# Kernel optimization log

Measured on AMD Instinct MI355X. Metric: run time of the kernel, lower is better.

## Reference

```python
import jax, jax.numpy as jnp
import numpy as np

N_NODES = 50000
N_EDGES = 800000
D = 128


def setup_inputs() -> dict:
    key = jax.random.key(0)
    ks = jax.random.split(key, 7)
    return {
        "shape_features": jax.random.normal(ks[0], (N_NODES, D), dtype=jnp.float32),
        "W1": jax.random.normal(ks[1], (D, D), dtype=jnp.float32) * 0.05,
        "b1": jax.random.normal(ks[2], (D,), dtype=jnp.float32) * 0.05,
        "W2": jax.random.normal(ks[3], (D, D), dtype=jnp.float32) * 0.05,
        "b2": jax.random.normal(ks[4], (D,), dtype=jnp.float32) * 0.05,
        "edge_src": jax.random.randint(ks[5], (N_EDGES,), 0, N_NODES, dtype=jnp.int32),
        "edge_dst": jax.random.randint(ks[6], (N_EDGES,), 0, N_NODES, dtype=jnp.int32),
    }


def reference(shape_features, W1, b1, W2, b2, edge_src, edge_dst):
    # out1 = linear1(x)  (torch Linear: x @ W.T + b)
    out1 = jnp.einsum("nd,od->no", shape_features, W1) + b1
    # ragged neighbour gather + sum per destination node (segment reduce)
    aggr = jax.ops.segment_sum(shape_features[edge_src], edge_dst,
                               num_segments=shape_features.shape[0])
    # out = linear1(x) + linear2(aggr)
    return out1 + jnp.einsum("nd,od->no", aggr, W2) + b2
```

## Files before the change

kernel.cpp:

```cpp
#include <hip/hip_runtime.h>
#include <hip/hip_bf16.h>

#define DF 128
#define BSH 5
#define BNODES 32
#define NBMAX 2048
#define PCHUNK 8192
#define BCHUNK 4096
#define TILE 2048
#define ASTRIDE 68
#define SRCMASK 0x07ffffffu

typedef __attribute__((ext_vector_type(8))) short short8;
typedef __attribute__((ext_vector_type(4))) float floatx4;

__device__ __forceinline__ ushort f2bf(float f) {
    __hip_bfloat16 h = __float2bfloat16(f);
    return *reinterpret_cast<ushort*>(&h);
}

__global__ __launch_bounds__(256) void prep_kernel(
    const float* __restrict__ x, ushort* __restrict__ xbf, int n4,
    const float* __restrict__ W1, const float* __restrict__ W2,
    const float* __restrict__ b1, const float* __restrict__ b2,
    ushort* __restrict__ w1bf, ushort* __restrict__ w2bf, float* __restrict__ bias,
    const int* __restrict__ dst, int* __restrict__ ghist, int* __restrict__ done,
    int* __restrict__ gbase, int* __restrict__ gcur,
    int n_edges, int PH, int nb)
{
    __shared__ int h[NBMAX];
    __shared__ int isLast;
    int bid = blockIdx.x;
    if (bid < PH) {
        for (int j = threadIdx.x; j < nb; j += 256) h[j] = 0;
        __syncthreads();
        int base = bid * PCHUNK;
#pragma unroll 4
        for (int i = 0; i < PCHUNK / 256; ++i) {
            int e = base + i * 256 + threadIdx.x;
            if (e < n_edges) atomicAdd(&h[dst[e] >> BSH], 1);
        }
        __syncthreads();
        for (int j = threadIdx.x; j < nb; j += 256) {
            int c = h[j];
            if (c) atomicAdd(&ghist[j], c);
        }
        __threadfence();
        __syncthreads();
        if (threadIdx.x == 0) isLast = (atomicAdd(done, 1) == PH - 1);
        __syncthreads();
        if (isLast) {
            int b0 = threadIdx.x * 8;
            int vals[8];
            int s = 0;
#pragma unroll
            for (int k = 0; k < 8; ++k) {
                int idx = b0 + k;
                int v = (idx < nb)
                    ? __hip_atomic_load(&ghist[idx], __ATOMIC_RELAXED,
                                        __HIP_MEMORY_SCOPE_AGENT)
                    : 0;
                vals[k] = v; s += v;
            }
            h[threadIdx.x] = s;
            __syncthreads();
            for (int off = 1; off < 256; off <<= 1) {
                int u = (threadIdx.x >= off) ? h[threadIdx.x - off] : 0;
                __syncthreads();
                h[threadIdx.x] += u;
                __syncthreads();
            }
            int run = h[threadIdx.x] - s;
#pragma unroll
            for (int k = 0; k < 8; ++k) {
                int idx = b0 + k;
                if (idx < nb) { gbase[idx] = run; gcur[idx] = run; run += vals[k]; }
            }
            if (threadIdx.x == 0) gbase[nb] = n_edges;
        }
    } else if (bid < PH + 64) {
        int i = (bid - PH) * 256 + threadIdx.x;
        if (i < DF * DF) {
            w1bf[i] = f2bf(W1[i]);
            w2bf[i] = f2bf(W2[i]);
        }
        if (i < DF) bias[i] = b1[i] + b2[i];
    } else {
        int i = (bid - PH - 64) * 256 + threadIdx.x;
        if (i < n4) {
            float4 v = reinterpret_cast<const float4*>(x)[i];
            ushort4 o;
            o.x = f2bf(v.x); o.y = f2bf(v.y); o.z = f2bf(v.z); o.w = f2bf(v.w);
            reinterpret_cast<ushort4*>(xbf)[i] = o;
        }
    }
}

__global__ __launch_bounds__(512) void bin_kernel(
    const int* __restrict__ src, const int* __restrict__ dst,
    int* __restrict__ gcur, uint* __restrict__ pairs, int n_edges, int nb)
{
    __shared__ int h[NBMAX];
    int tid = threadIdx.x;
    for (int j = tid; j < nb; j += 512) h[j] = 0;
    __syncthreads();
    int base = blockIdx.x * BCHUNK;
    int d[8], sv[8];
#pragma unroll
    for (int k = 0; k < 8; ++k) {
        int i = base + k * 512 + tid;
        bool ok = i < n_edges;
        d[k]  = ok ? dst[i] : -1;
        sv[k] = ok ? src[i] : 0;
        if (ok) atomicAdd(&h[d[k] >> BSH], 1);
    }
    __syncthreads();
    for (int j = tid; j < nb; j += 512) {
        int c = h[j];
        if (c) h[j] = atomicAdd(&gcur[j], c);
    }
    __syncthreads();
#pragma unroll
    for (int k = 0; k < 8; ++k) {
        if (d[k] >= 0) {
            int p = atomicAdd(&h[d[k] >> BSH], 1);
            pairs[p] = (uint)sv[k] | ((uint)(d[k] & (BNODES - 1)) << 27);
        }
    }
}

__global__ __launch_bounds__(256, 6) void agg_gemm_kernel(
    const ushort* __restrict__ xbf, const uint* __restrict__ pairs,
    const int* __restrict__ gbase,
    const ushort* __restrict__ w1, const ushort* __restrict__ w2,
    const float* __restrict__ bias, float* __restrict__ out, int n_nodes)
{
    __shared__ uint sorted[TILE];
    __shared__ uint abuf[BNODES * ASTRIDE];
    __shared__ int hcnt[BNODES];
    __shared__ int hoff[BNODES + 1];
    __shared__ int hcur[BNODES];

    int blk   = blockIdx.x;
    int node0 = blk * BNODES;
    int wave  = threadIdx.x >> 6;
    int lane  = threadIdx.x & 63;

    int start = gbase[blk];
    int end   = gbase[blk + 1];

    const char* xu = (const char*)xbf;
    uint lane4 = (uint)lane << 2;

    float2 acc[8];
#pragma unroll
    for (int i = 0; i < 8; ++i) acc[i] = make_float2(0.f, 0.f);

    for (int t0 = start; t0 < end; t0 += TILE) {
        int cnt = end - t0; if (cnt > TILE) cnt = TILE;

        if (threadIdx.x < BNODES) hcnt[threadIdx.x] = 0;
        __syncthreads();

        uint pk_[8];
#pragma unroll
        for (int k = 0; k < 8; ++k) {
            int i = threadIdx.x + k * 256;
            if (i < cnt) {
                uint pk = pairs[t0 + i];
                pk_[k] = pk;
                atomicAdd(&hcnt[pk >> 27], 1);
            }
        }
        __syncthreads();

        if (threadIdx.x < 64) {
            int v = (lane < BNODES) ? hcnt[lane] : 0;
#pragma unroll
            for (int off = 1; off < BNODES; off <<= 1) {
                int u = __shfl_up(v, off);
                if (lane >= off) v += u;
            }
            if (lane < BNODES) {
                hoff[lane + 1] = v;
                hcur[lane] = v - hcnt[lane];
            }
            if (lane == 0) hoff[0] = 0;
        }
        __syncthreads();

#pragma unroll
        for (int k = 0; k < 8; ++k) {
            int i = threadIdx.x + k * 256;
            if (i < cnt) {
                uint pk = pk_[k];
                int p = atomicAdd(&hcur[pk >> 27], 1);
                sorted[p] = (pk & SRCMASK) << 8;
            }
        }
        __syncthreads();

#pragma unroll
        for (int i = 0; i < 8; ++i) {
            int nl = wave * 8 + i;
            int j0 = hoff[nl], j1 = hoff[nl + 1];
            float2 a = acc[i];
            int j = j0;
            for (; j + 15 < j1; j += 16) {
                uint u[16];
#pragma unroll
                for (int k = 0; k < 16; ++k)
                    u[k] = *(const uint*)(xu + (size_t)(sorted[j + k] + lane4));
#pragma unroll
                for (int k = 0; k < 16; ++k) {
                    a.x += __uint_as_float(u[k] << 16);
                    a.y += __uint_as_float(u[k] & 0xffff0000u);
                }
            }
            for (; j + 3 < j1; j += 4) {
                uint u0 = *(const uint*)(xu + (size_t)(sorted[j + 0] + lane4));
                uint u1 = *(const uint*)(xu + (size_t)(sorted[j + 1] + lane4));
                uint u2 = *(const uint*)(xu + (size_t)(sorted[j + 2] + lane4));
                uint u3 = *(const uint*)(xu + (size_t)(sorted[j + 3] + lane4));
                a.x += __uint_as_float(u0 << 16) + __uint_as_float(u1 << 16)
                     + __uint_as_float(u2 << 16) + __uint_as_float(u3 << 16);
                a.y += __uint_as_float(u0 & 0xffff0000u) + __uint_as_float(u1 & 0xffff0000u)
                     + __uint_as_float(u2 & 0xffff0000u) + __uint_as_float(u3 & 0xffff0000u);
            }
            for (; j < j1; ++j) {
                uint u = *(const uint*)(xu + (size_t)(sorted[j] + lane4));
                a.x += __uint_as_float(u << 16);
                a.y += __uint_as_float(u & 0xffff0000u);
            }
            acc[i] = a;
        }
        __syncthreads();
    }

#pragma unroll
    for (int i = 0; i < 8; ++i) {
        int nl = wave * 8 + i;
        abuf[nl * ASTRIDE + lane] =
            (uint)f2bf(acc[i].x) | ((uint)f2bf(acc[i].y) << 16);
    }
    __syncthreads();

    int quad = lane >> 4;
    int m    = lane & 15;
    int rg   = wave >> 1;
    int half = wave & 1;
    int rowL = rg * 16 + m;
    int rowG = node0 + rowL;
    int rowC = (rowG < n_nodes) ? rowG : (n_nodes - 1);

    short8 xa[4], aa[4];
#pragma unroll
    for (int ks = 0; ks < 4; ++ks) {
        xa[ks] = *reinterpret_cast<const short8*>(xbf + (size_t)rowC * DF + ks * 32 + quad * 8);
        aa[ks] = *reinterpret_cast<const short8*>(&abuf[rowL * ASTRIDE + ks * 16 + quad * 4]);
    }

    int nbase = node0 + rg * 16;
#pragma unroll
    for (int oi = 0; oi < 4; ++oi) {
        int ot = half * 4 + oi;
        int o = ot * 16 + m;
        floatx4 c = {0.f, 0.f, 0.f, 0.f};
#pragma unroll
        for (int ks = 0; ks < 4; ++ks) {
            short8 bf1 = *reinterpret_cast<const short8*>(w1 + (size_t)o * DF + ks * 32 + quad * 8);
            short8 bf2 = *reinterpret_cast<const short8*>(w2 + (size_t)o * DF + ks * 32 + quad * 8);
            c = __builtin_amdgcn_mfma_f32_16x16x32_bf16(xa[ks], bf1, c, 0, 0, 0);
            c = __builtin_amdgcn_mfma_f32_16x16x32_bf16(aa[ks], bf2, c, 0, 0, 0);
        }
        float bv = bias[o];
#pragma unroll
        for (int r = 0; r < 4; ++r) {
            int row = nbase + quad * 4 + r;
            if (row < n_nodes) out[(size_t)row * DF + o] = c[r] + bv;
        }
    }
}

extern "C" void kernel_launch(void* const* d_in, const int* in_sizes, int n_in,
                              void* d_out, int out_size, void* d_ws, size_t ws_size,
                              hipStream_t stream) {
    const float* x  = (const float*)d_in[0];
    const float* W1 = (const float*)d_in[1];
    const float* b1 = (const float*)d_in[2];
    const float* W2 = (const float*)d_in[3];
    const float* b2 = (const float*)d_in[4];
    const int* esrc = (const int*)d_in[5];
    const int* edst = (const int*)d_in[6];
    float* out = (float*)d_out;

    int n_nodes = in_sizes[0] / DF;
    int n_edges = in_sizes[5];

    int nb = (n_nodes + BNODES - 1) >> BSH;
    int PH = (n_edges + PCHUNK - 1) / PCHUNK;
    int BB = (n_edges + BCHUNK - 1) / BCHUNK;

    char* ws = (char*)d_ws;
    ushort* xbf   = (ushort*)ws;                 ws += (size_t)n_nodes * DF * 2;
    ushort* w1bf  = (ushort*)ws;                 ws += (size_t)DF * DF * 2;
    ushort* w2bf  = (ushort*)ws;                 ws += (size_t)DF * DF * 2;
    float*  bias  = (float*)ws;                  ws += (size_t)DF * 4;
    int*    ghist = (int*)ws;                    ws += (size_t)(nb + 1) * 4;
    int*    done  = ghist + nb;
    int*    gbase = (int*)ws;                    ws += (size_t)(nb + 1) * 4;
    int*    gcur  = (int*)ws;                    ws += (size_t)nb * 4;
    uint*   pairs = (uint*)ws;

    hipMemsetAsync(ghist, 0, (size_t)(nb + 1) * sizeof(int), stream);

    int n4 = n_nodes * DF / 4;
    int prep_blocks = PH + 64 + (n4 + 255) / 256;
    prep_kernel<<<prep_blocks, 256, 0, stream>>>(
        x, xbf, n4, W1, W2, b1, b2, w1bf, w2bf, bias,
        edst, ghist, done, gbase, gcur, n_edges, PH, nb);

    bin_kernel<<<BB, 512, 0, stream>>>(esrc, edst, gcur, pairs, n_edges, nb);

    agg_gemm_kernel<<<nb, 256, 0, stream>>>(
        xbf, pairs, gbase, w1bf, w2bf, bias, out, n_nodes);
}
```

Baseline: 188.1 us.

## Two-level radix binning of edges and interleaved 4-node gather loop

Replaces the single scatter pass over 1563 fine bins with a two-level sort. The prep kernel first buckets edges into 49 coarse 1024-node chunks through a shared-memory staging buffer. A second kernel then sorts each chunk into 32 fine bins, so the scattered global writes become more coalesced. The aggregation loop now processes four nodes at once in batches of 8 with predicated loads, which raises memory-level parallelism at the cost of some wasted loads. Risks: src is packed into 16 bits (needs n_nodes < 65536), CAPC caps the per-chunk capacity, and NC_ is hardcoded to the node count.

```diff
diff --git a/kernel.cpp b/kernel.cpp
--- a/kernel.cpp
+++ b/kernel.cpp
@@ -5,8 +5,12 @@
 #define BSH 5
 #define BNODES 32
 #define NBMAX 2048
-#define PCHUNK 8192
-#define BCHUNK 4096
+#define CSH 10
+#define NC_ 49
+#define CAPC 24576
+#define PCHUNK 4096
+#define CHUNKB 4096
+#define KMAX 6
 #define TILE 2048
 #define ASTRIDE 68
 #define SRCMASK 0x07ffffffu
@@ -19,42 +23,96 @@
     return *reinterpret_cast<ushort*>(&h);
 }
 
-__global__ __launch_bounds__(256) void prep_kernel(
+__global__ __launch_bounds__(512) void prep_kernel(
     const float* __restrict__ x, ushort* __restrict__ xbf, int n4,
     const float* __restrict__ W1, const float* __restrict__ W2,
     const float* __restrict__ b1, const float* __restrict__ b2,
     ushort* __restrict__ w1bf, ushort* __restrict__ w2bf, float* __restrict__ bias,
-    const int* __restrict__ dst, int* __restrict__ ghist, int* __restrict__ done,
-    int* __restrict__ gbase, int* __restrict__ gcur,
-    int n_edges, int PH, int nb)
+    const int* __restrict__ src, const int* __restrict__ dst,
+    int* __restrict__ ghist, int* __restrict__ done, int* __restrict__ gcurC,
+    uint* __restrict__ stagingC, int* __restrict__ gbase, int* __restrict__ gcurF,
+    int n_edges, int EB, int WB, int nb)
 {
-    __shared__ int h[NBMAX];
-    __shared__ int isLast;
+    __shared__ int  hf[NBMAX];
+    __shared__ int  hc[NC_];
+    __shared__ int  lcur[NC_];
+    __shared__ int  wb[NC_];
+    __shared__ uint stg[PCHUNK];
+    __shared__ int  isLast;
+
     int bid = blockIdx.x;
-    if (bid < PH) {
-        for (int j = threadIdx.x; j < nb; j += 256) h[j] = 0;
-        __syncthreads();
+    int tid = threadIdx.x;
+
+    if (bid < EB) {
         int base = bid * PCHUNK;
-#pragma unroll 4
-        for (int i = 0; i < PCHUNK / 256; ++i) {
-            int e = base + i * 256 + threadIdx.x;
-            if (e < n_edges) atomicAdd(&h[dst[e] >> BSH], 1);
-        }
-        __syncthreads();
-        for (int j = threadIdx.x; j < nb; j += 256) {
-            int c = h[j];
+        int cnt = n_edges - base; if (cnt > PCHUNK) cnt = PCHUNK;
+
+        for (int j = tid; j < nb; j += 512) hf[j] = 0;
+        if (tid < NC_) hc[tid] = 0;
+        __syncthreads();
+#pragma unroll
+        for (int k = 0; k < PCHUNK / 512; ++k) {
+            int i = k * 512 + tid;
+            if (i < cnt) {
+                int d = dst[base + i];
+                atomicAdd(&hf[d >> BSH], 1);
+                atomicAdd(&hc[d >> CSH], 1);
+            }
+        }
+        __syncthreads();
+        for (int j = tid; j < nb; j += 512) {
+            int c = hf[j];
             if (c) atomicAdd(&ghist[j], c);
         }
+        if (tid < 64) {
+            int c = (tid < NC_) ? hc[tid] : 0;
+            int s = c;
+#pragma unroll
+            for (int off = 1; off < 64; off <<= 1) {
+                int u = __shfl_up(s, off);
+                if (tid >= off) s += u;
+            }
+            if (tid < NC_) {
+                int excl = s - c;
+                lcur[tid] = excl;
+                int gp = 0;
+                if (c > 0) gp = atomicAdd(&gcurC[tid], c);
+                wb[tid] = tid * CAPC + gp - excl;
+            }
+        }
+        __syncthreads();
+#pragma unroll
+        for (int k = 0; k < PCHUNK / 512; ++k) {
+            int i = k * 512 + tid;
+            if (i < cnt) {
+                int e = base + i;
+                int d = dst[e];
+                int c = d >> CSH;
+                uint pk = (uint)src[e] | ((uint)(d & 1023) << 16) | ((uint)c << 26);
+                int p = atomicAdd(&lcur[c], 1);
+                stg[p] = pk;
+            }
+        }
+        __syncthreads();
+#pragma unroll
+        for (int k = 0; k < PCHUNK / 512; ++k) {
+            int i = k * 512 + tid;
+            if (i < cnt) {
+                uint pk = stg[i];
+                int c = (int)(pk >> 26);
+                stagingC[wb[c] + i] = pk;
+            }
+        }
         __threadfence();
         __syncthreads();
-        if (threadIdx.x == 0) isLast = (atomicAdd(done, 1) == PH - 1);
+        if (tid == 0) isLast = (atomicAdd(done, 1) == EB - 1);
         __syncthreads();
         if (isLast) {
-            int b0 = threadIdx.x * 8;
-            int vals[8];
+            int b0 = tid * 4;
+            int vals[4];
             int s = 0;
 #pragma unroll
-            for (int k = 0; k < 8; ++k) {
+            for (int k = 0; k < 4; ++k) {
                 int idx = b0 + k;
                 int v = (idx < nb)
                     ? __hip_atomic_load(&ghist[idx], __ATOMIC_RELAXED,
@@ -62,31 +120,31 @@
                     : 0;
                 vals[k] = v; s += v;
             }
-            h[threadIdx.x] = s;
+            hf[tid] = s;
             __syncthreads();
-            for (int off = 1; off < 256; off <<= 1) {
-                int u = (threadIdx.x >= off) ? h[threadIdx.x - off] : 0;
+            for (int off = 1; off < 512; off <<= 1) {
+                int u = (tid >= off) ? hf[tid - off] : 0;
                 __syncthreads();
-                h[threadIdx.x] += u;
+                hf[tid] += u;
                 __syncthreads();
             }
-            int run = h[threadIdx.x] - s;
-#pragma unroll
-            for (int k = 0; k < 8; ++k) {
+            int run = hf[tid] - s;
+#pragma unroll
+            for (int k = 0; k < 4; ++k) {
                 int idx = b0 + k;
-                if (idx < nb) { gbase[idx] = run; gcur[idx] = run; run += vals[k]; }
-            }
-            if (threadIdx.x == 0) gbase[nb] = n_edges;
-        }
-    } else if (bid < PH + 64) {
-        int i = (bid - PH) * 256 + threadIdx.x;
+                if (idx < nb) { gbase[idx] = run; gcurF[idx] = run; run += vals[k]; }
+            }
+            if (tid == 0) gbase[nb] = n_edges;
+        }
+    } else if (bid < EB + WB) {
+        int i = (bid - EB) * 512 + tid;
         if (i < DF * DF) {
             w1bf[i] = f2bf(W1[i]);
             w2bf[i] = f2bf(W2[i]);
         }
         if (i < DF) bias[i] = b1[i] + b2[i];
     } else {
-        int i = (bid - PH - 64) * 256 + threadIdx.x;
+        int i = (bid - EB - WB) * 512 + tid;
         if (i < n4) {
             float4 v = reinterpret_cast<const float4*>(x)[i];
             ushort4 o;
@@ -96,35 +154,75 @@
     }
 }
 
-__global__ __launch_bounds__(512) void bin_kernel(
-    const int* __restrict__ src, const int* __restrict__ dst,
-    int* __restrict__ gcur, uint* __restrict__ pairs, int n_edges, int nb)
+__global__ __launch_bounds__(512) void binB_kernel(
+    const uint* __restrict__ stagingC, const int* __restrict__ gcurC,
+    int* __restrict__ gcurF, uint* __restrict__ pairs)
 {
-    __shared__ int h[NBMAX];
+    __shared__ uint stg[CHUNKB];
+    __shared__ int h32[BNODES];
+    __shared__ int lcur[BNODES];
+    __shared__ int wb[BNODES];
+
+    int c = blockIdx.x / KMAX;
+    int k = blockIdx.x % KMAX;
     int tid = threadIdx.x;
-    for (int j = tid; j < nb; j += 512) h[j] = 0;
+
+    int size = gcurC[c];
+    if (size > CAPC) size = CAPC;
+    int s0 = k * CHUNKB;
+    if (s0 >= size) return;
+    int cnt = size - s0; if (cnt > CHUNKB) cnt = CHUNKB;
+    const uint* sp = stagingC + (size_t)c * CAPC + s0;
+
+    if (tid < BNODES) h32[tid] = 0;
     __syncthreads();
-    int base = blockIdx.x * BCHUNK;
-    int d[8], sv[8];
-#pragma unroll
-    for (int k = 0; k < 8; ++k) {
-        int i = base + k * 512 + tid;
-        bool ok = i < n_edges;
-        d[k]  = ok ? dst[i] : -1;
-        sv[k] = ok ? src[i] : 0;
-        if (ok) atomicAdd(&h[d[k] >> BSH], 1);
+
+    uint mypk[CHUNKB / 512];
+#pragma unroll
+    for (int q = 0; q < CHUNKB / 512; ++q) {
+        int i = q * 512 + tid;
+        if (i < cnt) {
+            uint pk = sp[i];
+            mypk[q] = pk;
+            atomicAdd(&h32[(pk >> 21) & 31], 1);
+        }
     }
     __syncthreads();
-    for (int j = tid; j < nb; j += 512) {
-        int c = h[j];
-        if (c) h[j] = atomicAdd(&gcur[j], c);
+    if (tid < 64) {
+        int v = (tid < BNODES) ? h32[tid] : 0;
+        int s = v;
+#pragma unroll
+        for (int off = 1; off < BNODES; off <<= 1) {
+            int u = __shfl_up(s, off);
+            if (tid >= off) s += u;
+        }
+        if (tid < BNODES) {
+            int excl = s - v;
+            lcur[tid] = excl;
+            int gp = 0;
+            if (v > 0) gp = atomicAdd(&gcurF[c * BNODES + tid], v);
+            wb[tid] = gp - excl;
+        }
     }
     __syncthreads();
 #pragma unroll
-    for (int k = 0; k < 8; ++k) {
-        if (d[k] >= 0) {
-            int p = atomicAdd(&h[d[k] >> BSH], 1);
-            pairs[p] = (uint)sv[k] | ((uint)(d[k] & (BNODES - 1)) << 27);
+    for (int q = 0; q < CHUNKB / 512; ++q) {
+        int i = q * 512 + tid;
+        if (i < cnt) {
+            uint pk = mypk[q];
+            int p = atomicAdd(&lcur[(pk >> 21) & 31], 1);
+            stg[p] = pk;
+        }
+    }
+    __syncthreads();
+#pragma unroll
+    for (int q = 0; q < CHUNKB / 512; ++q) {
+        int i = q * 512 + tid;
+        if (i < cnt) {
+            uint pk = stg[i];
+            int f = (int)((pk >> 21) & 31);
+            uint out = (pk & 0xFFFFu) | (((pk >> 16) & 31u) << 27);
+            pairs[wb[f] + i] = out;
         }
     }
 }
@@ -200,39 +298,55 @@
         }
         __syncthreads();
 
-#pragma unroll
-        for (int i = 0; i < 8; ++i) {
-            int nl = wave * 8 + i;
-            int j0 = hoff[nl], j1 = hoff[nl + 1];
-            float2 a = acc[i];
-            int j = j0;
-            for (; j + 15 < j1; j += 16) {
-                uint u[16];
-#pragma unroll
-                for (int k = 0; k < 16; ++k)
-                    u[k] = *(const uint*)(xu + (size_t)(sorted[j + k] + lane4));
-#pragma unroll
-                for (int k = 0; k < 16; ++k) {
-                    a.x += __uint_as_float(u[k] << 16);
-                    a.y += __uint_as_float(u[k] & 0xffff0000u);
+        int hv[9];
+#pragma unroll
+        for (int q = 0; q <= 8; ++q) hv[q] = hoff[wave * 8 + q];
+        int safe = hv[0];
+#pragma unroll
+        for (int g = 0; g < 2; ++g) {
+            int j0 = hv[g * 4 + 0], e0 = hv[g * 4 + 1];
+            int j1 = e0,            e1 = hv[g * 4 + 2];
+            int j2 = e1,            e2 = hv[g * 4 + 3];
+            int j3 = e2,            e3 = hv[g * 4 + 4];
+            int rem = e0 - j0;
+            rem = max(rem, e1 - j1);
+            rem = max(rem, e2 - j2);
+            rem = max(rem, e3 - j3);
+            float2 a0 = acc[g * 4 + 0], a1 = acc[g * 4 + 1];
+            float2 a2 = acc[g * 4 + 2], a3 = acc[g * 4 + 3];
+            while (rem > 0) {
+                uint u0[8], u1[8], u2[8], u3[8];
+#pragma unroll
+                for (int k = 0; k < 8; ++k) {
+                    int i0 = (j0 + k < e0) ? j0 + k : safe;
+                    int i1 = (j1 + k < e1) ? j1 + k : safe;
+                    int i2 = (j2 + k < e2) ? j2 + k : safe;
+                    int i3 = (j3 + k < e3) ? j3 + k : safe;
+                    u0[k] = *(const uint*)(xu + (size_t)(sorted[i0] + lane4));
+                    u1[k] = *(const uint*)(xu + (size_t)(sorted[i1] + lane4));
+                    u2[k] = *(const uint*)(xu + (size_t)(sorted[i2] + lane4));
+                    u3[k] = *(const uint*)(xu + (size_t)(sorted[i3] + lane4));
                 }
-            }
-            for (; j + 3 < j1; j += 4) {
-                uint u0 = *(const uint*)(xu + (size_t)(sorted[j + 0] + lane4));
-                uint u1 = *(const uint*)(xu + (size_t)(sorted[j + 1] + lane4));
-                uint u2 = *(const uint*)(xu + (size_t)(sorted[j + 2] + lane4));
-                uint u3 = *(const uint*)(xu + (size_t)(sorted[j + 3] + lane4));
-                a.x += __uint_as_float(u0 << 16) + __uint_as_float(u1 << 16)
-                     + __uint_as_float(u2 << 16) + __uint_as_float(u3 << 16);
-                a.y += __uint_as_float(u0 & 0xffff0000u) + __uint_as_float(u1 & 0xffff0000u)
-                     + __uint_as_float(u2 & 0xffff0000u) + __uint_as_float(u3 & 0xffff0000u);
-            }
-            for (; j < j1; ++j) {
-                uint u = *(const uint*)(xu + (size_t)(sorted[j] + lane4));
-                a.x += __uint_as_float(u << 16);
-                a.y += __uint_as_float(u & 0xffff0000u);
-            }
-            acc[i] = a;
+#pragma unroll
+                for (int k = 0; k < 8; ++k) {
+                    uint v0 = (j0 + k < e0) ? u0[k] : 0u;
+                    uint v1 = (j1 + k < e1) ? u1[k] : 0u;
+                    uint v2 = (j2 + k < e2) ? u2[k] : 0u;
+                    uint v3 = (j3 + k < e3) ? u3[k] : 0u;
+                    a0.x += __uint_as_float(v0 << 16);
+                    a0.y += __uint_as_float(v0 & 0xffff0000u);
+                    a1.x += __uint_as_float(v1 << 16);
+                    a1.y += __uint_as_float(v1 & 0xffff0000u);
+                    a2.x += __uint_as_float(v2 << 16);
+                    a2.y += __uint_as_float(v2 & 0xffff0000u);
+                    a3.x += __uint_as_float(v3 << 16);
+                    a3.y += __uint_as_float(v3 & 0xffff0000u);
+                }
+                j0 += 8; j1 += 8; j2 += 8; j3 += 8;
+                rem -= 8;
+            }
+            acc[g * 4 + 0] = a0; acc[g * 4 + 1] = a1;
+            acc[g * 4 + 2] = a2; acc[g * 4 + 3] = a3;
         }
         __syncthreads();
     }
@@ -298,29 +412,32 @@
     int n_edges = in_sizes[5];
 
     int nb = (n_nodes + BNODES - 1) >> BSH;
-    int PH = (n_edges + PCHUNK - 1) / PCHUNK;
-    int BB = (n_edges + BCHUNK - 1) / BCHUNK;
+    int EB = (n_edges + PCHUNK - 1) / PCHUNK;
+    int WB = (DF * DF + 511) / 512;
 
     char* ws = (char*)d_ws;
-    ushort* xbf   = (ushort*)ws;                 ws += (size_t)n_nodes * DF * 2;
-    ushort* w1bf  = (ushort*)ws;                 ws += (size_t)DF * DF * 2;
-    ushort* w2bf  = (ushort*)ws;                 ws += (size_t)DF * DF * 2;
-    float*  bias  = (float*)ws;                  ws += (size_t)DF * 4;
-    int*    ghist = (int*)ws;                    ws += (size_t)(nb + 1) * 4;
-    int*    done  = ghist + nb;
-    int*    gbase = (int*)ws;                    ws += (size_t)(nb + 1) * 4;
-    int*    gcur  = (int*)ws;                    ws += (size_t)nb * 4;
-    uint*   pairs = (uint*)ws;
-
-    hipMemsetAsync(ghist, 0, (size_t)(nb + 1) * sizeof(int), stream);
+    ushort* xbf     = (ushort*)ws;               ws += (size_t)n_nodes * DF * 2;
+    ushort* w1bf    = (ushort*)ws;               ws += (size_t)DF * DF * 2;
+    ushort* w2bf    = (ushort*)ws;               ws += (size_t)DF * DF * 2;
+    float*  bias    = (float*)ws;                ws += (size_t)DF * 4;
+    int*    ghist   = (int*)ws;                  ws += (size_t)(nb + 1 + NC_) * 4;
+    int*    done    = ghist + nb;
+    int*    gcurC   = done + 1;
+    int*    gbase   = (int*)ws;                  ws += (size_t)(nb + 1) * 4;
+    int*    gcurF   = (int*)ws;                  ws += (size_t)nb * 4;
+    uint*   stagingC= (uint*)ws;                 ws += (size_t)NC_ * CAPC * 4;
+    uint*   pairs   = (uint*)ws;
+
+    hipMemsetAsync(ghist, 0, (size_t)(nb + 1 + NC_) * sizeof(int), stream);
 
     int n4 = n_nodes * DF / 4;
-    int prep_blocks = PH + 64 + (n4 + 255) / 256;
-    prep_kernel<<<prep_blocks, 256, 0, stream>>>(
+    int XB = (n4 + 511) / 512;
+    prep_kernel<<<EB + WB + XB, 512, 0, stream>>>(
         x, xbf, n4, W1, W2, b1, b2, w1bf, w2bf, bias,
-        edst, ghist, done, gbase, gcur, n_edges, PH, nb);
-
-    bin_kernel<<<BB, 512, 0, stream>>>(esrc, edst, gcur, pairs, n_edges, nb);
+        esrc, edst, ghist, done, gcurC, stagingC, gbase, gcurF,
+        n_edges, EB, WB, nb);
+
+    binB_kernel<<<NC_ * KMAX, 512, 0, stream>>>(stagingC, gcurC, gcurF, pairs);
 
     agg_gemm_kernel<<<nb, 256, 0, stream>>>(
         xbf, pairs, gbase, w1bf, w2bf, bias, out, n_nodes);
```

After: 211.3 us. +12.3%, slower.
